# Kernel optimization log

Hardware: AMD Instinct MI355X
Metric: run time of the kernel (lower is better)

## Reference

```python
import jax, jax.numpy as jnp
import numpy as np

BN_EPS = 1e-5


def _conv(x, w):
    # x: [N, Cin, H, W], w: [Cout, Cin, kh, kw], stride 1, padding 1 (same for 3x3)
    return jax.lax.conv_general_dilated(
        x, w, window_strides=(1, 1), padding=[(1, 1), (1, 1)],
        dimension_numbers=('NCHW', 'OIHW', 'NCHW'))


def setup_inputs() -> dict:
    key = jax.random.key(0)
    ks = jax.random.split(key, 4)
    T, N, Cin, Cout, H, W = 16, 4, 64, 64, 64, 64
    x = jax.random.normal(ks[0], (T, N, Cin, H, W), dtype=jnp.float32)
    # conv_x2h: Conv2d(Cin, 4*Cout, k=3, s=1, p=1, bias=True) + BatchNorm2d(4*Cout)
    Wx = jax.random.normal(ks[1], (4 * Cout, Cin, 3, 3), dtype=jnp.float32) * 0.05
    bx = jax.random.normal(ks[2], (4 * Cout,), dtype=jnp.float32) * 0.05
    gamma = jnp.ones((4 * Cout,), dtype=jnp.float32)
    beta = jnp.zeros((4 * Cout,), dtype=jnp.float32)
    # conv_h2h: Conv2d(Cout, 4*Cout, k=3, p=1, bias=False)
    Wh = jax.random.normal(ks[3], (4 * Cout, Cout, 3, 3), dtype=jnp.float32) * 0.05
    return {"x": x, "Wx": Wx, "bx": bx, "gamma": gamma, "beta": beta, "Wh": Wh}


def reference(x, Wx, bx, gamma, beta, Wh):
    T, N, Cin, H, W = x.shape
    hidden = Wh.shape[1]

    # ---- SequenceWise(Conv2d + BatchNorm(train) + Identity) ----
    xf = x.reshape(T * N, Cin, H, W)
    y = _conv(xf, Wx) + bx[None, :, None, None]
    mean = jnp.mean(y, axis=(0, 2, 3))
    var = jnp.var(y, axis=(0, 2, 3))  # biased, as torch BN uses for normalization
    y = (y - mean[None, :, None, None]) * jax.lax.rsqrt(var[None, :, None, None] + BN_EPS)
    y = y * gamma[None, :, None, None] + beta[None, :, None, None]
    y = y.reshape(T, N, 4 * hidden, H, W)

    # ---- ConvLSTMCell recurrence over time ----
    # zeros init is exactly equivalent to prev_h/prev_c = None:
    # conv_h2h(0) = 0 (no bias) and f*0 + i*g = i*g.
    h0 = jnp.zeros((N, hidden, H, W), dtype=x.dtype)
    c0 = jnp.zeros((N, hidden, H, W), dtype=x.dtype)

    def step(carry, xt):
        h, c = carry
        tmp = _conv(h, Wh) + xt
        cc_i, cc_f, cc_o, cc_g = jnp.split(tmp, 4, axis=1)
        i = jax.nn.sigmoid(cc_i)
        f = jax.nn.sigmoid(cc_f)
        o = jax.nn.sigmoid(cc_o)
        g = jnp.tanh(cc_g)
        c = f * c + i * g
        h = o * jnp.tanh(c)
        return (h, c), h

    _, hs = jax.lax.scan(step, (h0, c0), y)
    return hs  # [T, N, hidden, H, W]
```

## Files before the change

kernel.cpp:

```cpp
#include <hip/hip_runtime.h>
#include <hip/hip_bf16.h>

typedef float        f32x4  __attribute__((ext_vector_type(4)));
typedef unsigned int u32x4  __attribute__((ext_vector_type(4)));
typedef __bf16       bf16x8 __attribute__((ext_vector_type(8)));

__device__ __forceinline__ unsigned short f2bf(float f) {
    unsigned u = __builtin_bit_cast(unsigned, f);
    u += 0x7fffu + ((u >> 16) & 1u);
    return (unsigned short)(u >> 16);
}
__device__ __forceinline__ float bf2f(unsigned short u) {
    union { unsigned ui; float f; } c; c.ui = ((unsigned)u) << 16; return c.f;
}
__device__ __forceinline__ void gload_lds16(const void* g, void* l) {
    __builtin_amdgcn_global_load_lds(
        (const __attribute__((address_space(1))) unsigned int*)g,
        (__attribute__((address_space(3))) unsigned int*)l, 16, 0, 0);
}

__global__ __launch_bounds__(256) void k_xT(const float* __restrict__ x,
                                            unsigned short* __restrict__ xT) {
    __shared__ unsigned int tl[256 * 32];
    const int img = blockIdx.x >> 4;
    const int p0  = (blockIdx.x & 15) * 256;
    const int tid = threadIdx.x;
    const float* xi = x + (size_t)img * 64 * 4096 + p0 + tid;
#pragma unroll
    for (int cp = 0; cp < 32; ++cp) {
        float a = xi[(size_t)(2 * cp) * 4096];
        float b = xi[(size_t)(2 * cp + 1) * 4096];
        unsigned v = (unsigned)f2bf(a) | ((unsigned)f2bf(b) << 16);
        tl[tid * 32 + (cp ^ (tid & 31))] = v;
    }
    __syncthreads();
    unsigned short* dst = xT + ((size_t)img * 4096 + p0) * 64;
#pragma unroll
    for (int k = 0; k < 8; ++k) {
        int c = tid + k * 256;
        int pix = c >> 3, slot = c & 7;
        unsigned w[4];
#pragma unroll
        for (int i = 0; i < 4; ++i)
            w[i] = tl[pix * 32 + ((slot * 4 + i) ^ (pix & 31))];
        *(u32x4*)(dst + (size_t)pix * 64 + slot * 8) = *(u32x4*)w;
    }
}

__global__ __launch_bounds__(256) void k_pack(const float* __restrict__ W,
                                              unsigned short* __restrict__ Ap) {
    int idx = blockIdx.x * 256 + threadIdx.x;
    if (idx >= 256 * 576) return;
    int row = idx / 576, k = idx % 576;
    int kb = k / 288, r2 = k % 288;
    int tap = r2 / 32, w32 = r2 % 32;
    int s = w32 >> 3, e = w32 & 7;
    int ci = kb * 32 + ((s ^ (row & 3)) << 3) + e;
    int co = (row & 3) * 64 + (row >> 2);
    Ap[idx] = f2bf(W[((size_t)co * 64 + ci) * 9 + tap]);
}

__global__ __launch_bounds__(256) void k_conv0(
    const unsigned short* __restrict__ src,
    const unsigned short* __restrict__ Ap,
    unsigned short* __restrict__ ybf,
    float2* __restrict__ prt)
{
    constexpr int TH = 16, N_ = 4, HR = 18;

    __shared__ __align__(16) unsigned short halo[HR * 18 * 64];
    __shared__ __align__(16) unsigned short As[2][2048];

    const int bid  = blockIdx.x;
    const int xcd  = bid & 7;
    const int sidx = bid >> 3;
    const int grp  = sidx & 3;
    const int pairG = (sidx >> 2) * 8 + xcd;
    const int tile = pairG & 15;
    const int img  = pairG >> 4;
    const int py0 = (tile >> 2) * TH, px0 = (tile & 3) * 16;
    const int tid = threadIdx.x;
    const int wv = tid >> 6, lane = tid & 63;
    const int cl = lane & 15, q = lane >> 4;
    const int rowbase = grp * 64;

    f32x4 acc[4][N_];
#pragma unroll
    for (int m = 0; m < 4; ++m)
#pragma unroll
        for (int n = 0; n < N_; ++n)
            acc[m][n] = (f32x4){0.f, 0.f, 0.f, 0.f};

    {
        const char* agp = (const char*)Ap +
            (size_t)(rowbase + (tid >> 2)) * 1152 + (tid & 3) * 16;
        gload_lds16(agp, (char*)&As[0][0] + tid * 16);

        const unsigned short* sb = src + (size_t)img * 4096 * 64;
        char* hB = (char*)halo;
        for (int tau = tid; tau < HR * 144; tau += 256) {
            int s = tau & 7, hcc = (tau >> 3) % 18, hrr = tau / 144;
            int gy = py0 + hrr - 1, gx = px0 + hcc - 1;
            u32x4 v = {0u, 0u, 0u, 0u};
            if ((unsigned)gy < 64u && (unsigned)gx < 64u)
                v = *(const u32x4*)(sb + ((gy * 64 + gx) * 64 + s * 8));
            *(u32x4*)(hB + (hrr * 18 + hcc) * 128 + ((s * 16) ^ ((hcc & 7) << 4))) = v;
        }
        __syncthreads();

        int aoff[4];
#pragma unroll
        for (int m = 0; m < 4; ++m)
            aoff[m] = (m * 16 + cl) * 64 + ((q * 16) ^ ((cl & 3) << 4));

        const char* AsRd = (const char*)&As[0][0];
#pragma unroll
        for (int ks = 0; ks < 18; ++ks) {
            const int buf = ks & 1;
            if (ks < 17)
                gload_lds16(agp + (ks + 1) * 64, (char*)&As[buf ^ 1][0] + tid * 16);

            const int kb = ks / 9, tap = ks % 9;
            const int ky = tap / 3, kx = tap - ky * 3;

            u32x4 af[4];
#pragma unroll
            for (int m = 0; m < 4; ++m)
                af[m] = *(const u32x4*)(AsRd + buf * 4096 + aoff[m]);

            int hcv  = cl + kx;
            int cbase = hcv * 128 + ((kb * 64 + q * 16) ^ ((hcv & 7) << 4));
#pragma unroll
            for (int n = 0; n < N_; ++n) {
                int hr = wv * N_ + n + ky;
                u32x4 bv = *(const u32x4*)(hB + hr * 2304 + cbase);
                bf16x8 bfr = __builtin_bit_cast(bf16x8, bv);
#pragma unroll
                for (int m = 0; m < 4; ++m)
                    acc[m][n] = __builtin_amdgcn_mfma_f32_16x16x32_bf16(
                        __builtin_bit_cast(bf16x8, af[m]), bfr, acc[m][n], 0, 0, 0);
            }
            __syncthreads();
        }
    }

#pragma unroll
    for (int m = 0; m < 4; ++m) {
#pragma unroll
        for (int n = 0; n < N_; ++n) {
            int pix = (py0 + wv * N_ + n) * 64 + px0 + cl;
            uint2 w;
            w.x = (unsigned)f2bf(acc[m][n][0]) | ((unsigned)f2bf(acc[m][n][1]) << 16);
            w.y = (unsigned)f2bf(acc[m][n][2]) | ((unsigned)f2bf(acc[m][n][3]) << 16);
            *(uint2*)(ybf + ((size_t)img * 4096 + pix) * 256 + rowbase + m * 16 + q * 4) = w;
        }
    }
    float* bnred = (float*)halo;
#pragma unroll
    for (int m = 0; m < 4; ++m) {
#pragma unroll
        for (int j = 0; j < 4; ++j) {
            float s = 0.f, qq = 0.f;
#pragma unroll
            for (int n = 0; n < N_; ++n) {
                float v = acc[m][n][j];
                s += v; qq += v * v;
            }
#pragma unroll
            for (int mask = 1; mask <= 8; mask <<= 1) {
                s  += __shfl_xor(s,  mask, 64);
                qq += __shfl_xor(qq, mask, 64);
            }
            if (cl == 0) {
                int ci_ = (wv * 4 + q) * 16 + m * 4 + j;
                bnred[ci_ * 2]     = s;
                bnred[ci_ * 2 + 1] = qq;
            }
        }
    }
    __syncthreads();
    if (tid < 64) {
        int m_ = tid >> 4, qj = tid & 15;
        float s = 0.f, qq = 0.f;
#pragma unroll
        for (int w = 0; w < 4; ++w) {
            int idx = ((w * 4 + (qj >> 2)) * 16 + m_ * 4 + (qj & 3)) * 2;
            s += bnred[idx]; qq += bnred[idx + 1];
        }
        prt[(size_t)(rowbase + tid) * 1024 + img * 16 + tile] = make_float2(s, qq);
    }
}

__global__ __launch_bounds__(256) void k_bn_fin(
    const float2* __restrict__ prt, const float* __restrict__ bx,
    const float* __restrict__ gamma, const float* __restrict__ beta,
    float* __restrict__ ss) {
    int c = blockIdx.x;
    const float2* p = prt + (size_t)c * 1024;
    float s = 0.f, sq = 0.f;
    for (int i = threadIdx.x; i < 1024; i += 256) {
        float2 v = p[i]; s += v.x; sq += v.y;
    }
    __shared__ float rs[256], rq[256];
    int tid = threadIdx.x;
    rs[tid] = s; rq[tid] = sq;
    __syncthreads();
    for (int off = 128; off > 0; off >>= 1) {
        if (tid < off) { rs[tid] += rs[tid + off]; rq[tid] += rq[tid + off]; }
        __syncthreads();
    }
    if (tid == 0) {
        int co = (c & 3) * 64 + (c >> 2);
        float mean = rs[0] * (1.f / 262144.f);
        float var  = rq[0] * (1.f / 262144.f) - mean * mean;
        float sc   = gamma[co] * rsqrtf(var + 1e-5f);
        ss[c]       = sc;
        ss[256 + c] = beta[co] - mean * sc;
        (void)bx;
    }
}

__global__ __launch_bounds__(256) void k_step(
    const unsigned short* __restrict__ hin,
    const unsigned short* __restrict__ Ap,
    const unsigned short* __restrict__ ybf,
    const float* __restrict__ ss,
    float* __restrict__ cst,
    unsigned short* __restrict__ hout,
    float* __restrict__ out,
    int t, int first)
{
    constexpr int TH = 8, N_ = 2, HR = 10;

    __shared__ __align__(16) unsigned short halo[HR * 18 * 64];
    __shared__ __align__(16) unsigned short As[2][2048];

    const int bid  = blockIdx.x;
    const int xcd  = bid & 7;
    const int sidx = bid >> 3;
    const int grp  = sidx & 3;
    const int pairG = (sidx >> 2) * 8 + xcd;
    const int tile = pairG & 31;
    const int img  = pairG >> 5;
    const int py0 = (tile >> 2) * TH, px0 = (tile & 3) * 16;
    const int tid = threadIdx.x;
    const int wv = tid >> 6, lane = tid & 63;
    const int cl = lane & 15, q = lane >> 4;
    const int rowbase = grp * 64;

    uint2 ypre[4][N_];
    float cpre[4][N_];
#pragma unroll
    for (int m = 0; m < 4; ++m) {
        int hc = grp * 16 + m * 4 + q;
#pragma unroll
        for (int n = 0; n < N_; ++n) {
            int pix = (py0 + wv * N_ + n) * 64 + px0 + cl;
            ypre[m][n] = *(const uint2*)(ybf +
                ((size_t)(t * 4 + img) * 4096 + pix) * 256 + hc * 4);
            cpre[m][n] = first ? 0.f : cst[((size_t)img * 64 + hc) * 4096 + pix];
        }
    }

    f32x4 acc[4][N_];
#pragma unroll
    for (int m = 0; m < 4; ++m)
#pragma unroll
        for (int n = 0; n < N_; ++n)
            acc[m][n] = (f32x4){0.f, 0.f, 0.f, 0.f};

    if (!first) {
        const char* agp = (const char*)Ap +
            (size_t)(rowbase + (tid >> 2)) * 1152 + (tid & 3) * 16;
        gload_lds16(agp, (char*)&As[0][0] + tid * 16);

        const unsigned short* sb = hin + (size_t)img * 4096 * 64;
        char* hB = (char*)halo;
        for (int tau = tid; tau < HR * 144; tau += 256) {
            int s = tau & 7, hcc = (tau >> 3) % 18, hrr = tau / 144;
            int gy = py0 + hrr - 1, gx = px0 + hcc - 1;
            u32x4 v = {0u, 0u, 0u, 0u};
            if ((unsigned)gy < 64u && (unsigned)gx < 64u)
                v = *(const u32x4*)(sb + ((gy * 64 + gx) * 64 + s * 8));
            *(u32x4*)(hB + (hrr * 18 + hcc) * 128 + ((s * 16) ^ ((hcc & 7) << 4))) = v;
        }
        __syncthreads();

        int aoff[4];
#pragma unroll
        for (int m = 0; m < 4; ++m)
            aoff[m] = (m * 16 + cl) * 64 + ((q * 16) ^ ((cl & 3) << 4));

        const char* AsRd = (const char*)&As[0][0];
#pragma unroll
        for (int ks = 0; ks < 18; ++ks) {
            const int buf = ks & 1;
            if (ks < 17)
                gload_lds16(agp + (ks + 1) * 64, (char*)&As[buf ^ 1][0] + tid * 16);

            const int kb = ks / 9, tap = ks % 9;
            const int ky = tap / 3, kx = tap - ky * 3;

            u32x4 af[4];
#pragma unroll
            for (int m = 0; m < 4; ++m)
                af[m] = *(const u32x4*)(AsRd + buf * 4096 + aoff[m]);

            int hcv  = cl + kx;
            int cbase = hcv * 128 + ((kb * 64 + q * 16) ^ ((hcv & 7) << 4));
#pragma unroll
            for (int n = 0; n < N_; ++n) {
                int hr = wv * N_ + n + ky;
                u32x4 bv = *(const u32x4*)(hB + hr * 2304 + cbase);
                bf16x8 bfr = __builtin_bit_cast(bf16x8, bv);
#pragma unroll
                for (int m = 0; m < 4; ++m)
                    acc[m][n] = __builtin_amdgcn_mfma_f32_16x16x32_bf16(
                        __builtin_bit_cast(bf16x8, af[m]), bfr, acc[m][n], 0, 0, 0);
            }
            __syncthreads();
        }
    }

    unsigned short* hbounce = halo;
    const f32x4* sc4 = (const f32x4*)ss;
    const f32x4* sh4 = (const f32x4*)(ss + 256);
#pragma unroll
    for (int m = 0; m < 4; ++m) {
        int hc = grp * 16 + m * 4 + q;
        f32x4 sc = sc4[hc], sh = sh4[hc];
#pragma unroll
        for (int n = 0; n < N_; ++n) {
            int pix = (py0 + wv * N_ + n) * 64 + px0 + cl;
            uint2 yv = ypre[m][n];
            float tmp[4];
            tmp[0] = acc[m][n][0] + sc[0] * bf2f((unsigned short)(yv.x & 0xffffu)) + sh[0];
            tmp[1] = acc[m][n][1] + sc[1] * bf2f((unsigned short)(yv.x >> 16))     + sh[1];
            tmp[2] = acc[m][n][2] + sc[2] * bf2f((unsigned short)(yv.y & 0xffffu)) + sh[2];
            tmp[3] = acc[m][n][3] + sc[3] * bf2f((unsigned short)(yv.y >> 16))     + sh[3];
            float iv = 1.f / (1.f + __expf(-tmp[0]));
            float fv = 1.f / (1.f + __expf(-tmp[1]));
            float ov = 1.f / (1.f + __expf(-tmp[2]));
            float e2 = __expf(2.f * tmp[3]);
            float gv = 1.f - 2.f / (e2 + 1.f);
            size_t cidx = ((size_t)img * 64 + hc) * 4096 + pix;
            float cnew = fv * cpre[m][n] + iv * gv;
            cst[cidx] = cnew;
            float e2c = __expf(2.f * cnew);
            float hv  = ov * (1.f - 2.f / (e2c + 1.f));
            out[((size_t)(t * 4 + img) * 64 + hc) * 4096 + pix] = hv;
            hbounce[((wv * N_ + n) * 16 + cl) * 16 + m * 4 + q] = f2bf(hv);
        }
    }
    __syncthreads();
    if (tid < TH * 16) {
        int pixg = (py0 + (tid >> 4)) * 64 + px0 + (tid & 15);
        u32x4* dst = (u32x4*)(hout + ((size_t)img * 4096 + pixg) * 64 + grp * 16);
        u32x4* s0  = (u32x4*)(hbounce + tid * 16);
        dst[0] = s0[0];
        dst[1] = s0[1];
    }
}

extern "C" void kernel_launch(void* const* d_in, const int* in_sizes, int n_in,
                              void* d_out, int out_size, void* d_ws, size_t ws_size,
                              hipStream_t stream) {
    const float* x     = (const float*)d_in[0];
    const float* Wx    = (const float*)d_in[1];
    const float* bx    = (const float*)d_in[2];
    const float* gamma = (const float*)d_in[3];
    const float* beta  = (const float*)d_in[4];
    const float* Wh    = (const float*)d_in[5];
    float* out = (float*)d_out;

    char* ws = (char*)d_ws;
    unsigned short* y   = (unsigned short*)ws;
    unsigned short* Axp = (unsigned short*)(ws + 134217728);
    unsigned short* Ahp = (unsigned short*)(ws + 134512640);
    float*          ss  = (float*)(ws + 134807552);
    float*          cs  = (float*)(ws + 134809600);
    float2*         prt = (float2*)(ws + 139003904);
    unsigned short* hA  = (unsigned short*)(ws + 139003904);
    unsigned short* hB  = (unsigned short*)(ws + 141101056);

    unsigned short* xT = (unsigned short*)d_out;

    k_xT  <<<1024, 256, 0, stream>>>(x, xT);
    k_pack<<< 576, 256, 0, stream>>>(Wx, Axp);
    k_pack<<< 576, 256, 0, stream>>>(Wh, Ahp);

    k_conv0<<<4096, 256, 0, stream>>>(xT, Axp, y, prt);
    k_bn_fin<<<256, 256, 0, stream>>>(prt, bx, gamma, beta, ss);

    unsigned short* hbuf[2] = {hA, hB};
    for (int t = 0; t < 16; ++t) {
        k_step<<<512, 256, 0, stream>>>(hbuf[t & 1], Ahp, y, ss, cs,
                                        hbuf[(t + 1) & 1], out, t, t == 0 ? 1 : 0);
    }
}
```

Measured before the change: 382.7 us.

## Fuse LSTM timesteps into one persistent kernel with neighbor-tile flag sync

Replaces the 16 per-timestep kernel launches with a single persistent kernel that loops over time. Each block keeps its cell state in registers instead of round-tripping it through global memory. Blocks wait only on the spin flags of the 3x3 neighborhood of tiles whose hidden state they read, rather than on a full-grid barrier at each kernel boundary. This depends on all 512 blocks being co-resident, and it carries a risk of hangs or subtle memory-ordering races on the double-buffered h arrays.

Result: slower. 747.5 us (+95.3%).

```diff
diff --git a/kernel.cpp b/kernel.cpp
--- a/kernel.cpp
+++ b/kernel.cpp
@@ -220,15 +220,14 @@
     }
 }
 
-__global__ __launch_bounds__(256) void k_step(
-    const unsigned short* __restrict__ hin,
+__global__ __launch_bounds__(256) void k_steps(
     const unsigned short* __restrict__ Ap,
     const unsigned short* __restrict__ ybf,
     const float* __restrict__ ss,
-    float* __restrict__ cst,
-    unsigned short* __restrict__ hout,
+    unsigned short* __restrict__ hA,
+    unsigned short* __restrict__ hB,
     float* __restrict__ out,
-    int t, int first)
+    int* __restrict__ flags)
 {
     constexpr int TH = 8, N_ = 2, HR = 10;
 
@@ -247,9 +246,34 @@
     const int wv = tid >> 6, lane = tid & 63;
     const int cl = lane & 15, q = lane >> 4;
     const int rowbase = grp * 64;
+    const int ty = tile >> 2, tx = tile & 3;
+    const int fidx = (img * 32 + tile) * 16;
+
+    int nbr = -1;
+    if (tid < 9) {
+        int nty = ty + tid / 3 - 1, ntx = tx + tid % 3 - 1;
+        if ((unsigned)nty < 8u && (unsigned)ntx < 4u)
+            nbr = (img * 32 + nty * 4 + ntx) * 16;
+    }
+
+    const f32x4* sc4 = (const f32x4*)ss;
+    const f32x4* sh4 = (const f32x4*)(ss + 256);
+
+    int aoff[4];
+#pragma unroll
+    for (int m = 0; m < 4; ++m)
+        aoff[m] = (m * 16 + cl) * 64 + ((q * 16) ^ ((cl & 3) << 4));
+
+    const char* agp = (const char*)Ap +
+        (size_t)(rowbase + (tid >> 2)) * 1152 + (tid & 3) * 16;
+
+    float creg[4][N_];
+#pragma unroll
+    for (int m = 0; m < 4; ++m)
+#pragma unroll
+        for (int n = 0; n < N_; ++n) creg[m][n] = 0.f;
 
     uint2 ypre[4][N_];
-    float cpre[4][N_];
 #pragma unroll
     for (int m = 0; m < 4; ++m) {
         int hc = grp * 16 + m * 4 + q;
@@ -257,108 +281,128 @@
         for (int n = 0; n < N_; ++n) {
             int pix = (py0 + wv * N_ + n) * 64 + px0 + cl;
             ypre[m][n] = *(const uint2*)(ybf +
-                ((size_t)(t * 4 + img) * 4096 + pix) * 256 + hc * 4);
-            cpre[m][n] = first ? 0.f : cst[((size_t)img * 64 + hc) * 4096 + pix];
-        }
-    }
-
-    f32x4 acc[4][N_];
-#pragma unroll
-    for (int m = 0; m < 4; ++m)
-#pragma unroll
-        for (int n = 0; n < N_; ++n)
-            acc[m][n] = (f32x4){0.f, 0.f, 0.f, 0.f};
-
-    if (!first) {
-        const char* agp = (const char*)Ap +
-            (size_t)(rowbase + (tid >> 2)) * 1152 + (tid & 3) * 16;
-        gload_lds16(agp, (char*)&As[0][0] + tid * 16);
-
-        const unsigned short* sb = hin + (size_t)img * 4096 * 64;
-        char* hB = (char*)halo;
-        for (int tau = tid; tau < HR * 144; tau += 256) {
-            int s = tau & 7, hcc = (tau >> 3) % 18, hrr = tau / 144;
-            int gy = py0 + hrr - 1, gx = px0 + hcc - 1;
-            u32x4 v = {0u, 0u, 0u, 0u};
-            if ((unsigned)gy < 64u && (unsigned)gx < 64u)
-                v = *(const u32x4*)(sb + ((gy * 64 + gx) * 64 + s * 8));
-            *(u32x4*)(hB + (hrr * 18 + hcc) * 128 + ((s * 16) ^ ((hcc & 7) << 4))) = v;
+                ((size_t)img * 4096 + pix) * 256 + hc * 4);
+        }
+    }
+
+#pragma unroll 1
+    for (int t = 0; t < 16; ++t) {
+        const unsigned short* hin = (t & 1) ? hB : hA;
+        unsigned short*      hnxt = (t & 1) ? hA : hB;
+
+        f32x4 acc[4][N_];
+#pragma unroll
+        for (int m = 0; m < 4; ++m)
+#pragma unroll
+            for (int n = 0; n < N_; ++n)
+                acc[m][n] = (f32x4){0.f, 0.f, 0.f, 0.f};
+
+        if (t > 0) {
+            if (nbr >= 0) {
+                const int tgt = 4 * t;
+                while (__hip_atomic_load(flags + nbr, __ATOMIC_RELAXED,
+                                         __HIP_MEMORY_SCOPE_AGENT) < tgt)
+                    __builtin_amdgcn_s_sleep(2);
+                __threadfence();
+            }
+            __syncthreads();
+
+            gload_lds16(agp, (char*)&As[0][0] + tid * 16);
+            const unsigned short* sb = hin + (size_t)img * 4096 * 64;
+            char* hBp = (char*)halo;
+            for (int tau = tid; tau < HR * 144; tau += 256) {
+                int s = tau & 7, hcc = (tau >> 3) % 18, hrr = tau / 144;
+                int gy = py0 + hrr - 1, gx = px0 + hcc - 1;
+                u32x4 v = {0u, 0u, 0u, 0u};
+                if ((unsigned)gy < 64u && (unsigned)gx < 64u)
+                    v = *(const u32x4*)(sb + ((gy * 64 + gx) * 64 + s * 8));
+                *(u32x4*)(hBp + (hrr * 18 + hcc) * 128 + ((s * 16) ^ ((hcc & 7) << 4))) = v;
+            }
+            __syncthreads();
+
+            const char* AsRd = (const char*)&As[0][0];
+#pragma unroll
+            for (int ks = 0; ks < 18; ++ks) {
+                const int buf = ks & 1;
+                if (ks < 17)
+                    gload_lds16(agp + (ks + 1) * 64, (char*)&As[buf ^ 1][0] + tid * 16);
+
+                const int kb = ks / 9, tap = ks % 9;
+                const int ky = tap / 3, kx = tap - ky * 3;
+
+                u32x4 af[4];
+#pragma unroll
+                for (int m = 0; m < 4; ++m)
+                    af[m] = *(const u32x4*)(AsRd + buf * 4096 + aoff[m]);
+
+                int hcv  = cl + kx;
+                int cbase = hcv * 128 + ((kb * 64 + q * 16) ^ ((hcv & 7) << 4));
+#pragma unroll
+                for (int n = 0; n < N_; ++n) {
+                    int hr = wv * N_ + n + ky;
+                    u32x4 bv = *(const u32x4*)(hBp + hr * 2304 + cbase);
+                    bf16x8 bfr = __builtin_bit_cast(bf16x8, bv);
+#pragma unroll
+                    for (int m = 0; m < 4; ++m)
+                        acc[m][n] = __builtin_amdgcn_mfma_f32_16x16x32_bf16(
+                            __builtin_bit_cast(bf16x8, af[m]), bfr, acc[m][n], 0, 0, 0);
+                }
+                __syncthreads();
+            }
+        }
+
+        unsigned short* hbounce = halo;
+#pragma unroll
+        for (int m = 0; m < 4; ++m) {
+            int hc = grp * 16 + m * 4 + q;
+            f32x4 sc = sc4[hc], sh = sh4[hc];
+#pragma unroll
+            for (int n = 0; n < N_; ++n) {
+                int pix = (py0 + wv * N_ + n) * 64 + px0 + cl;
+                uint2 yv = ypre[m][n];
+                float tmp[4];
+                tmp[0] = acc[m][n][0] + sc[0] * bf2f((unsigned short)(yv.x & 0xffffu)) + sh[0];
+                tmp[1] = acc[m][n][1] + sc[1] * bf2f((unsigned short)(yv.x >> 16))     + sh[1];
+                tmp[2] = acc[m][n][2] + sc[2] * bf2f((unsigned short)(yv.y & 0xffffu)) + sh[2];
+                tmp[3] = acc[m][n][3] + sc[3] * bf2f((unsigned short)(yv.y >> 16))     + sh[3];
+                float iv = 1.f / (1.f + __expf(-tmp[0]));
+                float fv = 1.f / (1.f + __expf(-tmp[1]));
+                float ov = 1.f / (1.f + __expf(-tmp[2]));
+                float e2 = __expf(2.f * tmp[3]);
+                float gv = 1.f - 2.f / (e2 + 1.f);
+                float cnew = fv * creg[m][n] + iv * gv;
+                creg[m][n] = cnew;
+                float e2c = __expf(2.f * cnew);
+                float hv  = ov * (1.f - 2.f / (e2c + 1.f));
+                out[((size_t)(t * 4 + img) * 64 + hc) * 4096 + pix] = hv;
+                hbounce[((wv * N_ + n) * 16 + cl) * 16 + m * 4 + q] = f2bf(hv);
+            }
         }
         __syncthreads();
-
-        int aoff[4];
-#pragma unroll
-        for (int m = 0; m < 4; ++m)
-            aoff[m] = (m * 16 + cl) * 64 + ((q * 16) ^ ((cl & 3) << 4));
-
-        const char* AsRd = (const char*)&As[0][0];
-#pragma unroll
-        for (int ks = 0; ks < 18; ++ks) {
-            const int buf = ks & 1;
-            if (ks < 17)
-                gload_lds16(agp + (ks + 1) * 64, (char*)&As[buf ^ 1][0] + tid * 16);
-
-            const int kb = ks / 9, tap = ks % 9;
-            const int ky = tap / 3, kx = tap - ky * 3;
-
-            u32x4 af[4];
-#pragma unroll
-            for (int m = 0; m < 4; ++m)
-                af[m] = *(const u32x4*)(AsRd + buf * 4096 + aoff[m]);
-
-            int hcv  = cl + kx;
-            int cbase = hcv * 128 + ((kb * 64 + q * 16) ^ ((hcv & 7) << 4));
-#pragma unroll
-            for (int n = 0; n < N_; ++n) {
-                int hr = wv * N_ + n + ky;
-                u32x4 bv = *(const u32x4*)(hB + hr * 2304 + cbase);
-                bf16x8 bfr = __builtin_bit_cast(bf16x8, bv);
-#pragma unroll
-                for (int m = 0; m < 4; ++m)
-                    acc[m][n] = __builtin_amdgcn_mfma_f32_16x16x32_bf16(
-                        __builtin_bit_cast(bf16x8, af[m]), bfr, acc[m][n], 0, 0, 0);
-            }
-            __syncthreads();
-        }
-    }
-
-    unsigned short* hbounce = halo;
-    const f32x4* sc4 = (const f32x4*)ss;
-    const f32x4* sh4 = (const f32x4*)(ss + 256);
-#pragma unroll
-    for (int m = 0; m < 4; ++m) {
-        int hc = grp * 16 + m * 4 + q;
-        f32x4 sc = sc4[hc], sh = sh4[hc];
-#pragma unroll
-        for (int n = 0; n < N_; ++n) {
-            int pix = (py0 + wv * N_ + n) * 64 + px0 + cl;
-            uint2 yv = ypre[m][n];
-            float tmp[4];
-            tmp[0] = acc[m][n][0] + sc[0] * bf2f((unsigned short)(yv.x & 0xffffu)) + sh[0];
-            tmp[1] = acc[m][n][1] + sc[1] * bf2f((unsigned short)(yv.x >> 16))     + sh[1];
-            tmp[2] = acc[m][n][2] + sc[2] * bf2f((unsigned short)(yv.y & 0xffffu)) + sh[2];
-            tmp[3] = acc[m][n][3] + sc[3] * bf2f((unsigned short)(yv.y >> 16))     + sh[3];
-            float iv = 1.f / (1.f + __expf(-tmp[0]));
-            float fv = 1.f / (1.f + __expf(-tmp[1]));
-            float ov = 1.f / (1.f + __expf(-tmp[2]));
-            float e2 = __expf(2.f * tmp[3]);
-            float gv = 1.f - 2.f / (e2 + 1.f);
-            size_t cidx = ((size_t)img * 64 + hc) * 4096 + pix;
-            float cnew = fv * cpre[m][n] + iv * gv;
-            cst[cidx] = cnew;
-            float e2c = __expf(2.f * cnew);
-            float hv  = ov * (1.f - 2.f / (e2c + 1.f));
-            out[((size_t)(t * 4 + img) * 64 + hc) * 4096 + pix] = hv;
-            hbounce[((wv * N_ + n) * 16 + cl) * 16 + m * 4 + q] = f2bf(hv);
-        }
-    }
-    __syncthreads();
-    if (tid < TH * 16) {
-        int pixg = (py0 + (tid >> 4)) * 64 + px0 + (tid & 15);
-        u32x4* dst = (u32x4*)(hout + ((size_t)img * 4096 + pixg) * 64 + grp * 16);
-        u32x4* s0  = (u32x4*)(hbounce + tid * 16);
-        dst[0] = s0[0];
-        dst[1] = s0[1];
+        if (tid < TH * 16) {
+            int pixg = (py0 + (tid >> 4)) * 64 + px0 + (tid & 15);
+            u32x4* dst = (u32x4*)(hnxt + ((size_t)img * 4096 + pixg) * 64 + grp * 16);
+            u32x4* s0  = (u32x4*)(hbounce + tid * 16);
+            dst[0] = s0[0];
+            dst[1] = s0[1];
+        }
+        __syncthreads();
+        if (t < 15) {
+            if (tid == 0) {
+                __threadfence();
+                atomicAdd(flags + fidx, 1);
+            }
+#pragma unroll
+            for (int m = 0; m < 4; ++m) {
+                int hc = grp * 16 + m * 4 + q;
+#pragma unroll
+                for (int n = 0; n < N_; ++n) {
+                    int pix = (py0 + wv * N_ + n) * 64 + px0 + cl;
+                    ypre[m][n] = *(const uint2*)(ybf +
+                        ((size_t)((t + 1) * 4 + img) * 4096 + pix) * 256 + hc * 4);
+                }
+            }
+        }
     }
 }
 
@@ -378,7 +422,7 @@
     unsigned short* Axp = (unsigned short*)(ws + 134217728);
     unsigned short* Ahp = (unsigned short*)(ws + 134512640);
     float*          ss  = (float*)(ws + 134807552);
-    float*          cs  = (float*)(ws + 134809600);
+    int*            flg = (int*)(ws + 134809600);
     float2*         prt = (float2*)(ws + 139003904);
     unsigned short* hA  = (unsigned short*)(ws + 139003904);
     unsigned short* hB  = (unsigned short*)(ws + 141101056);
@@ -388,13 +432,10 @@
     k_xT  <<<1024, 256, 0, stream>>>(x, xT);
     k_pack<<< 576, 256, 0, stream>>>(Wx, Axp);
     k_pack<<< 576, 256, 0, stream>>>(Wh, Ahp);
+    hipMemsetAsync(flg, 0, 8192, stream);
 
     k_conv0<<<4096, 256, 0, stream>>>(xT, Axp, y, prt);
     k_bn_fin<<<256, 256, 0, stream>>>(prt, bx, gamma, beta, ss);
 
-    unsigned short* hbuf[2] = {hA, hB};
-    for (int t = 0; t < 16; ++t) {
-        k_step<<<512, 256, 0, stream>>>(hbuf[t & 1], Ahp, y, ss, cs,
-                                        hbuf[(t + 1) & 1], out, t, t == 0 ? 1 : 0);
-    }
-}
+    k_steps<<<512, 256, 0, stream>>>(Ahp, y, ss, hA, hB, out, flg);
+}
```
